# Optimization experiments

Measured on AMD Instinct MI355X. Metric: run time of the kernel, lower is better.

The kernel has to match this reference:

```python
import jax, jax.numpy as jnp
import numpy as np

EMBED_DIM = 512
N_HEADS = 8
HEAD_DIM = EMBED_DIM // N_HEADS
SEQ = 4096
BATCH = 2


def setup_inputs() -> dict:
    key = jax.random.key(0)
    k1, k2, k3 = jax.random.split(key, 3)
    x = jax.random.normal(k1, (SEQ, BATCH, EMBED_DIM), dtype=jnp.float32)
    # xavier_uniform for [3E, E]: limit = sqrt(6/(3E+E))
    lim_in = float(np.sqrt(6.0 / (3 * EMBED_DIM + EMBED_DIM)))
    in_proj_weight = jax.random.uniform(k2, (3 * EMBED_DIM, EMBED_DIM), minval=-lim_in, maxval=lim_in, dtype=jnp.float32)
    in_proj_bias = jnp.zeros((3 * EMBED_DIM,), jnp.float32)
    lim_out = float(np.sqrt(1.0 / EMBED_DIM))  # torch Linear default init range
    out_weight = jax.random.uniform(k3, (EMBED_DIM, EMBED_DIM), minval=-lim_out, maxval=lim_out, dtype=jnp.float32)
    out_bias = jnp.zeros((EMBED_DIM,), jnp.float32)
    return {"x": x, "in_proj_weight": in_proj_weight, "in_proj_bias": in_proj_bias,
            "out_weight": out_weight, "out_bias": out_bias}


def reference(x, in_proj_weight, in_proj_bias, out_weight, out_bias):
    # x: [S, B, E] (seq-first, as in the torch module)
    S, B, E = x.shape
    H, D = N_HEADS, HEAD_DIM
    scaling = 1.0 / (D ** 0.5)
    qkv = x @ in_proj_weight.T + in_proj_bias            # [S, B, 3E]
    q, k, v = jnp.split(qkv, 3, axis=-1)                 # each [S, B, E]
    # reshape to [B*H, S, D]
    def to_bh(t):
        return t.reshape(S, B * H, D).transpose(1, 0, 2)
    q = to_bh(q * scaling)
    k = to_bh(k)
    v = to_bh(v)
    scores = jnp.einsum('bqd,bkd->bqk', q, k)            # [B*H, S, S]
    attn = jax.nn.softmax(scores, axis=-1)
    out = jnp.einsum('bqk,bkd->bqd', attn, v)            # [B*H, S, D]
    out = out.transpose(1, 0, 2).reshape(S, B, E)        # [S, B, E]
    return out @ out_weight.T + out_bias
```

## Files before the change

kernel.cpp:

```cpp
#include <hip/hip_runtime.h>

typedef unsigned short u16;
typedef unsigned int   u32;
typedef short bf16x8 __attribute__((ext_vector_type(8)));
typedef float f32x2  __attribute__((ext_vector_type(2)));
typedef float f32x4  __attribute__((ext_vector_type(4)));
typedef float f32x16 __attribute__((ext_vector_type(16)));
typedef u32   u32x4  __attribute__((ext_vector_type(4)));

#define QK_SCALE 0.18033688011112042f

__device__ __forceinline__ u16 f2bf(float f) {
  u32 u = __builtin_bit_cast(u32, f);
  u = (u + 0x7FFFu + ((u >> 16) & 1u)) >> 16;
  return (u16)u;
}

__device__ __forceinline__ u32 cvtpk(float lo, float hi) {
  u32 r;
  asm("v_cvt_pk_bf16_f32 %0, %1, %2" : "=v"(r) : "v"(lo), "v"(hi));
  return r;
}

__device__ __forceinline__ void gload16(void* lds, const void* g) {
  __builtin_amdgcn_global_load_lds(
      (const __attribute__((address_space(1))) u32*)g,
      (__attribute__((address_space(3))) u32*)lds, 16, 0, 0);
}

__device__ __forceinline__ bf16x8 ld8(const void* p) {
  return *(const bf16x8*)p;
}

__global__ __launch_bounds__(256) void cvt_kernel(
    const float* __restrict__ x, const float* __restrict__ w1,
    const float* __restrict__ w2,
    u16* __restrict__ xb, u16* __restrict__ wb, u16* __restrict__ ob) {
  int i = blockIdx.x * 256 + threadIdx.x;
  const float* src; u16* dst; int off;
  if (i < 1048576)            { src = x;  dst = xb; off = i; }
  else if (i < 1048576+196608){ src = w1; dst = wb; off = i - 1048576; }
  else                        { src = w2; dst = ob; off = i - 1245184; }
  float4 v = ((const float4*)src)[off];
  ushort4 o;
  o.x = f2bf(v.x); o.y = f2bf(v.y); o.z = f2bf(v.z); o.w = f2bf(v.w);
  ((ushort4*)dst)[off] = o;
}

template<int MODE>
__global__ __launch_bounds__(256, 2) void gemm_bt(
    const u16* __restrict__ A, const u16* __restrict__ Bm,
    const float* __restrict__ bias,
    u16* __restrict__ q_out, u16* __restrict__ k_out, u16* __restrict__ v_out,
    float* __restrict__ f_out, int M, int N, int K) {
  __shared__ __attribute__((aligned(16))) u16 As[128 * 64];
  __shared__ __attribute__((aligned(16))) u16 Bs[128 * 64];
  const int tid = threadIdx.x, lane = tid & 63, w = tid >> 6;
  const int wm = w >> 1, wn = w & 1;
  const int lo = lane & 15, hi = lane >> 4;
  const int m0 = blockIdx.x * 128, n0 = blockIdx.y * 128;
  f32x4 acc[4][4] = {};
  const int srow = lane >> 3;
  const int skc  = (lane & 7) ^ srow;
  const int nk = K >> 6;
  for (int kt = 0; kt < nk; ++kt) {
    __syncthreads();
    const int k0 = kt * 64;
#pragma unroll
    for (int c = 0; c < 4; ++c) {
      const int ch = w * 4 + c;
      const int row = ch * 8 + srow;
      gload16((char*)As + ch * 1024, A  + (size_t)(m0 + row) * K + k0 + skc * 8);
      gload16((char*)Bs + ch * 1024, Bm + (size_t)(n0 + row) * K + k0 + skc * 8);
    }
    __syncthreads();
#pragma unroll
    for (int kk = 0; kk < 2; ++kk) {
      bf16x8 af[4], bfr[4];
#pragma unroll
      for (int mi = 0; mi < 4; ++mi) {
        const int row = wm * 64 + mi * 16 + lo;
        const int kc = kk * 4 + hi;
        af[mi] = ld8((const char*)As + row * 128 + ((kc ^ (row & 7)) << 4));
      }
#pragma unroll
      for (int ni = 0; ni < 4; ++ni) {
        const int row = wn * 64 + ni * 16 + lo;
        const int kc = kk * 4 + hi;
        bfr[ni] = ld8((const char*)Bs + row * 128 + ((kc ^ (row & 7)) << 4));
      }
#pragma unroll
      for (int mi = 0; mi < 4; ++mi)
#pragma unroll
        for (int ni = 0; ni < 4; ++ni)
          acc[mi][ni] = __builtin_amdgcn_mfma_f32_16x16x32_bf16(
              af[mi], bfr[ni], acc[mi][ni], 0, 0, 0);
    }
  }
#pragma unroll
  for (int mi = 0; mi < 4; ++mi)
#pragma unroll
    for (int ni = 0; ni < 4; ++ni) {
      const int gn = n0 + wn * 64 + ni * 16 + lo;
      const float bv = bias[gn];
#pragma unroll
      for (int r = 0; r < 4; ++r) {
        const int gm = m0 + wm * 64 + mi * 16 + hi * 4 + r;
        float val = acc[mi][ni][r] + bv;
        if (MODE == 0) {
          const int s = gm >> 1, b = gm & 1;
          const int sec = gn >> 9, e = gn & 511;
          const int h = e >> 6, d = e & 63;
          const size_t o = (((size_t)(b * 8 + h) * 4096 + s) << 6) + d;
          if (sec == 0)      q_out[o] = f2bf(val * QK_SCALE);
          else if (sec == 1) k_out[o] = f2bf(val);
          else               v_out[o] = f2bf(val);
        } else {
          f_out[(size_t)gm * N + gn] = val;
        }
      }
    }
}

__global__ __launch_bounds__(256) void transpose_v(
    const u16* __restrict__ v, u16* __restrict__ vt) {
  __shared__ __attribute__((aligned(16))) u16 T[64 * 72];
  const int bh = blockIdx.y, s0 = blockIdx.x * 64;
  const int t = threadIdx.x;
#pragma unroll
  for (int i = 0; i < 2; ++i) {
    const int idx = t + i * 256;
    const int row = idx >> 3, c = idx & 7;
    uint4 d = *(const uint4*)(v + ((size_t)bh * 4096 + s0 + row) * 64 + c * 8);
    *(uint4*)(&T[row * 72 + c * 8]) = d;
  }
  __syncthreads();
#pragma unroll
  for (int i = 0; i < 2; ++i) {
    const int idx = t + i * 256;
    const int dcol = idx >> 3, sc = idx & 7;
    u16 tmp[8];
#pragma unroll
    for (int j = 0; j < 8; ++j) tmp[j] = T[(sc * 8 + j) * 72 + dcol];
    *(uint4*)(vt + ((size_t)bh * 64 + dcol) * 4096 + s0 + sc * 8) = *(const uint4*)tmp;
  }
}

__global__ __launch_bounds__(256, 2) void fa_kernel(
    const u16* __restrict__ q, const u16* __restrict__ k,
    const u16* __restrict__ vt, u16* __restrict__ attn) {
  __shared__ __attribute__((aligned(16))) char S_lds[2][2][16384];
  __shared__ float Ml[2][2][32];
  const int tid = threadIdx.x, lane = tid & 63, w = tid >> 6;
  const int lo = lane & 31, hi5 = lane >> 5;
  const int wq = w & 1;
  const int kvh = w >> 1;
  const int wg = blockIdx.x;
  const int xcd = wg & 7, idx = wg >> 3;
  const int bh = xcd * 2 + (idx >> 5), qb = idx & 31;
  const int q0 = qb * 128 + wq * 64;
  const size_t hb = (size_t)bh * 4096 * 64;
  const u16* kbase = k + hb;
  const u16* vbase = vt + hb;
  bf16x8 qfA[4], qfB[4];
#pragma unroll
  for (int ds = 0; ds < 4; ++ds) {
    qfA[ds] = ld8(q + hb + (size_t)(q0 + lo) * 64 + ds * 16 + hi5 * 8);
    qfB[ds] = ld8(q + hb + (size_t)(q0 + 32 + lo) * 64 + ds * 16 + hi5 * 8);
  }

  f32x16 accA[2] = {}, accB[2] = {};
  float lrunA = 0.f, lrunB = 0.f;
  bf16x8 paA[4], paB[4];
  bf16x8 vfr[8];

  const int srow8 = lane >> 3;
  const int sx    = (lane & 7) ^ srow8;
  const int schunk = wq * 4;

#define STAGE(buf, kv0)                                                       \
  {                                                                           \
    char* kb_l = S_lds[kvh][buf];                                             \
    char* vb_l = kb_l + 8192;                                                 \
    _Pragma("unroll")                                                         \
    for (int i = 0; i < 4; ++i) {                                             \
      const int c = schunk + i;                       \
      gload16(kb_l + c * 1024,                                                \
              kbase + (size_t)((kv0) + c * 8 + srow8) * 64 + sx * 8);         \
      gload16(vb_l + c * 1024,                                                \
              vbase + (size_t)(c * 8 + srow8) * 4096 + (kv0) + sx * 8);       \
    }                                                                         \
  }

#define PACK(stv, ksl, pa)                                                    \
  {                                                                           \
    u32 A0 = cvtpk(stv[8 * ksl + 0], stv[8 * ksl + 1]);                       \
    u32 A1 = cvtpk(stv[8 * ksl + 2], stv[8 * ksl + 3]);                       \
    u32 B0 = cvtpk(stv[8 * ksl + 4], stv[8 * ksl + 5]);                       \
    u32 B1 = cvtpk(stv[8 * ksl + 6], stv[8 * ksl + 7]);                       \
    asm("v_permlane32_swap_b32 %0, %1" : "+v"(A0), "+v"(B0));                 \
    asm("v_permlane32_swap_b32 %0, %1" : "+v"(A1), "+v"(B1));                 \
    u32x4 pw; pw.x = A0; pw.y = A1; pw.z = B0; pw.w = B1;                     \
    pa = __builtin_bit_cast(bf16x8, pw);                                      \
  }

#define PVSTEP()                                                              \
  {                                                                           \
    __builtin_amdgcn_s_setprio(1);                                            \
    _Pragma("unroll")                                                         \
    for (int sl = 0; sl < 4; ++sl)                                            \
      _Pragma("unroll")                                                       \
      for (int ds2 = 0; ds2 < 2; ++ds2) {                                     \
        accA[ds2] = __builtin_amdgcn_mfma_f32_32x32x16_bf16(                  \
            paA[sl], vfr[sl * 2 + ds2], accA[ds2], 0, 0, 0);                  \
        accB[ds2] = __builtin_amdgcn_mfma_f32_32x32x16_bf16(                  \
            paB[sl], vfr[sl * 2 + ds2], accB[ds2], 0, 0, 0);                  \
      }                                                                       \
    __builtin_amdgcn_s_setprio(0);                                            \
  }

#define COMPUTE(CUR)                                                          \
  {                                                                           \
    const char* kl = S_lds[kvh][CUR];                                         \
    const char* vl = kl + 8192;                                               \
    f32x16 stA0 = {}, stA1 = {}, stB0 = {}, stB1 = {};                        \
    __builtin_amdgcn_s_setprio(1);                                            \
    _Pragma("unroll")                                                         \
    for (int ds = 0; ds < 4; ++ds) {                                          \
      const int r0 = lo, r1 = 32 + lo;                                        \
      const int col = ds * 32 + hi5 * 16;                                     \
      bf16x8 kf0 = ld8(kl + r0 * 128 + (col ^ ((r0 & 7) << 4)));              \
      bf16x8 kf1 = ld8(kl + r1 * 128 + (col ^ ((r1 & 7) << 4)));              \
      stA0 = __builtin_amdgcn_mfma_f32_32x32x16_bf16(kf0, qfA[ds], stA0,0,0,0);\
      stB0 = __builtin_amdgcn_mfma_f32_32x32x16_bf16(kf0, qfB[ds], stB0,0,0,0);\
      stA1 = __builtin_amdgcn_mfma_f32_32x32x16_bf16(kf1, qfA[ds], stA1,0,0,0);\
      stB1 = __builtin_amdgcn_mfma_f32_32x32x16_bf16(kf1, qfB[ds], stB1,0,0,0);\
    }                                                                         \
    __builtin_amdgcn_s_setprio(0);                                            \
    _Pragma("unroll")                                                         \
    for (int sl = 0; sl < 4; ++sl)                                            \
      _Pragma("unroll")                                                       \
      for (int ds2 = 0; ds2 < 2; ++ds2) {                                     \
        const int row = ds2 * 32 + lo;                                        \
        vfr[sl * 2 + ds2] = ld8(vl + row * 128 +                              \
                                ((sl * 32 + hi5 * 16) ^ ((row & 7) << 4)));   \
      }                                                                       \
    f32x2 ltA; ltA.x = 0.f; ltA.y = 0.f;                                      \
    f32x2 ltB; ltB.x = 0.f; ltB.y = 0.f;                                      \
    _Pragma("unroll")                                                         \
    for (int i = 0; i < 8; ++i) {                                             \
      stA0[2*i]   = __builtin_amdgcn_exp2f(stA0[2*i]);                        \
      stA0[2*i+1] = __builtin_amdgcn_exp2f(stA0[2*i+1]);                      \
      f32x2 a0; a0.x = stA0[2*i]; a0.y = stA0[2*i+1]; ltA += a0;              \
      stA1[2*i]   = __builtin_amdgcn_exp2f(stA1[2*i]);                        \
      stA1[2*i+1] = __builtin_amdgcn_exp2f(stA1[2*i+1]);                      \
      f32x2 a1; a1.x = stA1[2*i]; a1.y = stA1[2*i+1]; ltA += a1;              \
      stB0[2*i]   = __builtin_amdgcn_exp2f(stB0[2*i]);                        \
      stB0[2*i+1] = __builtin_amdgcn_exp2f(stB0[2*i+1]);                      \
      f32x2 b0; b0.x = stB0[2*i]; b0.y = stB0[2*i+1]; ltB += b0;              \
      stB1[2*i]   = __builtin_amdgcn_exp2f(stB1[2*i]);                        \
      stB1[2*i+1] = __builtin_amdgcn_exp2f(stB1[2*i+1]);                      \
      f32x2 b1; b1.x = stB1[2*i]; b1.y = stB1[2*i+1]; ltB += b1;              \
    }                                                                         \
    lrunA += ltA.x + ltA.y;                                                   \
    lrunB += ltB.x + ltB.y;                                                   \
    PACK(stA0, 0, paA[0]); PACK(stA0, 1, paA[1]);                             \
    PACK(stA1, 0, paA[2]); PACK(stA1, 1, paA[3]);                             \
    PACK(stB0, 0, paB[0]); PACK(stB0, 1, paB[1]);                             \
    PACK(stB1, 0, paB[2]); PACK(stB1, 1, paB[3]);                             \
  }

  const int kvbase = kvh * 2048;
  STAGE(0, kvbase);
  __syncthreads();
  STAGE(1, kvbase + 64);
  COMPUTE(0);
  __syncthreads();

  for (int t = 1; t < 32; ++t) {
    const int cur = t & 1;
    if (t < 31) STAGE(cur ^ 1, kvbase + (t + 1) * 64);
    PVSTEP();
    if (cur) { COMPUTE(1); } else { COMPUTE(0); }
    __syncthreads();
  }
  PVSTEP();

  lrunA += __shfl_xor(lrunA, 32);
  lrunB += __shfl_xor(lrunB, 32);
  float* Ob = (float*)S_lds;
  if (w >= 2) {
#pragma unroll
    for (int r = 0; r < 16; ++r) {
      const int crow = (r & 3) + 8 * (r >> 2) + 4 * hi5;
#pragma unroll
      for (int ds2 = 0; ds2 < 2; ++ds2) {
        Ob[((wq * 2 + 0) * 32 + crow) * 64 + ds2 * 32 + lo] = accA[ds2][r];
        Ob[((wq * 2 + 1) * 32 + crow) * 64 + ds2 * 32 + lo] = accB[ds2][r];
      }
    }
    if (hi5 == 0) { Ml[wq][0][lo] = lrunA; Ml[wq][1][lo] = lrunB; }
  }
  __syncthreads();
  if (w < 2) {
    const float linvA = 1.0f / (lrunA + Ml[wq][0][lo]);
    const float linvB = 1.0f / (lrunB + Ml[wq][1][lo]);
    const int b = bh >> 3, h = bh & 7;
#pragma unroll
    for (int r = 0; r < 16; ++r) {
      const int crow = (r & 3) + 8 * (r >> 2) + 4 * hi5;
      const float ivA = __shfl(linvA, crow);
      const float ivB = __shfl(linvB, crow);
      const int sA = q0 + crow, sB = q0 + 32 + crow;
#pragma unroll
      for (int ds2 = 0; ds2 < 2; ++ds2) {
        const float oA = Ob[((wq * 2 + 0) * 32 + crow) * 64 + ds2 * 32 + lo];
        const float oB = Ob[((wq * 2 + 1) * 32 + crow) * 64 + ds2 * 32 + lo];
        attn[(size_t)(sA * 2 + b) * 512 + h * 64 + ds2 * 32 + lo] =
            f2bf((accA[ds2][r] + oA) * ivA);
        attn[(size_t)(sB * 2 + b) * 512 + h * 64 + ds2 * 32 + lo] =
            f2bf((accB[ds2][r] + oB) * ivB);
      }
    }
  }
#undef STAGE
#undef PACK
#undef PVSTEP
#undef COMPUTE
}

extern "C" void kernel_launch(void* const* d_in, const int* in_sizes, int n_in,
                              void* d_out, int out_size, void* d_ws, size_t ws_size,
                              hipStream_t stream) {
  const float* x     = (const float*)d_in[0];
  const float* w_in  = (const float*)d_in[1];
  const float* b_in  = (const float*)d_in[2];
  const float* w_out = (const float*)d_in[3];
  const float* b_out = (const float*)d_in[4];
  float* out = (float*)d_out;
  char* ws = (char*)d_ws;
  u16* xb  = (u16*)(ws);
  u16* wb  = (u16*)(ws + 8388608);
  u16* ob  = (u16*)(ws + 9961472);
  u16* qb  = (u16*)(ws + 10485760);
  u16* kb  = (u16*)(ws + 18874368);
  u16* vb  = (u16*)(ws + 27262976);
  u16* vtb = (u16*)(ws + 35651584);
  u16* attn = xb;

  cvt_kernel<<<5120, 256, 0, stream>>>(x, w_in, w_out, xb, wb, ob);
  gemm_bt<0><<<dim3(64, 12), 256, 0, stream>>>(xb, wb, b_in, qb, kb, vb,
                                               nullptr, 8192, 1536, 512);
  transpose_v<<<dim3(64, 16), 256, 0, stream>>>(vb, vtb);
  fa_kernel<<<512, 256, 0, stream>>>(qb, kb, vtb, attn);
  gemm_bt<1><<<dim3(64, 4), 256, 0, stream>>>(attn, ob, b_out, nullptr, nullptr,
                                              nullptr, out, 8192, 512, 512);
}
```

Baseline: 132.4 us.

## Halve FA query tile per wave and ping-pong two score tiles across KV steps

The attention kernel now gives each wave 32 query rows instead of 64 and doubles the grid to 1024 workgroups. The main loop alternates between even and odd score/V-fragment register sets, so the QK^T MFMAs for the next KV block can overlap the exp/pack/PV work of the previous one. The aim is better occupancy and latency hiding. In exchange, each K/V tile staged in LDS is reused by half as many query rows, which doubles K/V global traffic. An extra barrier is also added before the epilogue reuses LDS.

```diff
diff --git a/kernel.cpp b/kernel.cpp
--- a/kernel.cpp
+++ b/kernel.cpp
@@ -31,6 +31,8 @@
 __device__ __forceinline__ bf16x8 ld8(const void* p) {
   return *(const bf16x8*)p;
 }
+
+__device__ __forceinline__ f32x16 fz16() { f32x16 z = {}; return z; }
 
 __global__ __launch_bounds__(256) void cvt_kernel(
     const float* __restrict__ x, const float* __restrict__ w1,
@@ -150,29 +152,27 @@
     const u16* __restrict__ q, const u16* __restrict__ k,
     const u16* __restrict__ vt, u16* __restrict__ attn) {
   __shared__ __attribute__((aligned(16))) char S_lds[2][2][16384];
-  __shared__ float Ml[2][2][32];
+  __shared__ float Ml[2][32];
   const int tid = threadIdx.x, lane = tid & 63, w = tid >> 6;
   const int lo = lane & 31, hi5 = lane >> 5;
   const int wq = w & 1;
   const int kvh = w >> 1;
   const int wg = blockIdx.x;
   const int xcd = wg & 7, idx = wg >> 3;
-  const int bh = xcd * 2 + (idx >> 5), qb = idx & 31;
-  const int q0 = qb * 128 + wq * 64;
+  const int bh = xcd * 2 + (idx >> 6), qb = idx & 63;
+  const int q0 = qb * 64 + wq * 32;
   const size_t hb = (size_t)bh * 4096 * 64;
   const u16* kbase = k + hb;
   const u16* vbase = vt + hb;
-  bf16x8 qfA[4], qfB[4];
-#pragma unroll
-  for (int ds = 0; ds < 4; ++ds) {
-    qfA[ds] = ld8(q + hb + (size_t)(q0 + lo) * 64 + ds * 16 + hi5 * 8);
-    qfB[ds] = ld8(q + hb + (size_t)(q0 + 32 + lo) * 64 + ds * 16 + hi5 * 8);
-  }
-
-  f32x16 accA[2] = {}, accB[2] = {};
-  float lrunA = 0.f, lrunB = 0.f;
-  bf16x8 paA[4], paB[4];
-  bf16x8 vfr[8];
+  bf16x8 qf[4];
+#pragma unroll
+  for (int ds = 0; ds < 4; ++ds)
+    qf[ds] = ld8(q + hb + (size_t)(q0 + lo) * 64 + ds * 16 + hi5 * 8);
+
+  f32x16 acc[2] = {};
+  float lrun = 0.f;
+  f32x16 stE0, stE1, stO0, stO1;
+  bf16x8 vfE[8], vfO[8];
 
   const int srow8 = lane >> 3;
   const int sx    = (lane & 7) ^ srow8;
@@ -204,129 +204,116 @@
     pa = __builtin_bit_cast(bf16x8, pw);                                      \
   }
 
-#define PVSTEP()                                                              \
-  {                                                                           \
-    __builtin_amdgcn_s_setprio(1);                                            \
-    _Pragma("unroll")                                                         \
-    for (int sl = 0; sl < 4; ++sl)                                            \
-      _Pragma("unroll")                                                       \
-      for (int ds2 = 0; ds2 < 2; ++ds2) {                                     \
-        accA[ds2] = __builtin_amdgcn_mfma_f32_32x32x16_bf16(                  \
-            paA[sl], vfr[sl * 2 + ds2], accA[ds2], 0, 0, 0);                  \
-        accB[ds2] = __builtin_amdgcn_mfma_f32_32x32x16_bf16(                  \
-            paB[sl], vfr[sl * 2 + ds2], accB[ds2], 0, 0, 0);                  \
-      }                                                                       \
-    __builtin_amdgcn_s_setprio(0);                                            \
-  }
-
-#define COMPUTE(CUR)                                                          \
+#define PRODUCE(CUR, S0, S1, VF)                                              \
   {                                                                           \
     const char* kl = S_lds[kvh][CUR];                                         \
     const char* vl = kl + 8192;                                               \
-    f32x16 stA0 = {}, stA1 = {}, stB0 = {}, stB1 = {};                        \
-    __builtin_amdgcn_s_setprio(1);                                            \
+    S0 = fz16(); S1 = fz16();                                                 \
     _Pragma("unroll")                                                         \
     for (int ds = 0; ds < 4; ++ds) {                                          \
       const int r0 = lo, r1 = 32 + lo;                                        \
       const int col = ds * 32 + hi5 * 16;                                     \
       bf16x8 kf0 = ld8(kl + r0 * 128 + (col ^ ((r0 & 7) << 4)));              \
       bf16x8 kf1 = ld8(kl + r1 * 128 + (col ^ ((r1 & 7) << 4)));              \
-      stA0 = __builtin_amdgcn_mfma_f32_32x32x16_bf16(kf0, qfA[ds], stA0,0,0,0);\
-      stB0 = __builtin_amdgcn_mfma_f32_32x32x16_bf16(kf0, qfB[ds], stB0,0,0,0);\
-      stA1 = __builtin_amdgcn_mfma_f32_32x32x16_bf16(kf1, qfA[ds], stA1,0,0,0);\
-      stB1 = __builtin_amdgcn_mfma_f32_32x32x16_bf16(kf1, qfB[ds], stB1,0,0,0);\
+      S0 = __builtin_amdgcn_mfma_f32_32x32x16_bf16(kf0, qf[ds], S0, 0, 0, 0); \
+      S1 = __builtin_amdgcn_mfma_f32_32x32x16_bf16(kf1, qf[ds], S1, 0, 0, 0); \
     }                                                                         \
-    __builtin_amdgcn_s_setprio(0);                                            \
     _Pragma("unroll")                                                         \
     for (int sl = 0; sl < 4; ++sl)                                            \
       _Pragma("unroll")                                                       \
       for (int ds2 = 0; ds2 < 2; ++ds2) {                                     \
         const int row = ds2 * 32 + lo;                                        \
-        vfr[sl * 2 + ds2] = ld8(vl + row * 128 +                              \
-                                ((sl * 32 + hi5 * 16) ^ ((row & 7) << 4)));   \
+        VF[sl * 2 + ds2] = ld8(vl + row * 128 +                               \
+                               ((sl * 32 + hi5 * 16) ^ ((row & 7) << 4)));    \
       }                                                                       \
-    f32x2 ltA; ltA.x = 0.f; ltA.y = 0.f;                                      \
-    f32x2 ltB; ltB.x = 0.f; ltB.y = 0.f;                                      \
+  }
+
+#define CONSUME(S0, S1, VF)                                                   \
+  {                                                                           \
+    f32x2 lt; lt.x = 0.f; lt.y = 0.f;                                         \
     _Pragma("unroll")                                                         \
     for (int i = 0; i < 8; ++i) {                                             \
-      stA0[2*i]   = __builtin_amdgcn_exp2f(stA0[2*i]);                        \
-      stA0[2*i+1] = __builtin_amdgcn_exp2f(stA0[2*i+1]);                      \
-      f32x2 a0; a0.x = stA0[2*i]; a0.y = stA0[2*i+1]; ltA += a0;              \
-      stA1[2*i]   = __builtin_amdgcn_exp2f(stA1[2*i]);                        \
-      stA1[2*i+1] = __builtin_amdgcn_exp2f(stA1[2*i+1]);                      \
-      f32x2 a1; a1.x = stA1[2*i]; a1.y = stA1[2*i+1]; ltA += a1;              \
-      stB0[2*i]   = __builtin_amdgcn_exp2f(stB0[2*i]);                        \
-      stB0[2*i+1] = __builtin_amdgcn_exp2f(stB0[2*i+1]);                      \
-      f32x2 b0; b0.x = stB0[2*i]; b0.y = stB0[2*i+1]; ltB += b0;              \
-      stB1[2*i]   = __builtin_amdgcn_exp2f(stB1[2*i]);                        \
-      stB1[2*i+1] = __builtin_amdgcn_exp2f(stB1[2*i+1]);                      \
-      f32x2 b1; b1.x = stB1[2*i]; b1.y = stB1[2*i+1]; ltB += b1;              \
+      S0[2*i]   = __builtin_amdgcn_exp2f(S0[2*i]);                            \
+      S0[2*i+1] = __builtin_amdgcn_exp2f(S0[2*i+1]);                          \
+      f32x2 e0; e0.x = S0[2*i]; e0.y = S0[2*i+1]; lt += e0;                   \
+      S1[2*i]   = __builtin_amdgcn_exp2f(S1[2*i]);                            \
+      S1[2*i+1] = __builtin_amdgcn_exp2f(S1[2*i+1]);                          \
+      f32x2 e1; e1.x = S1[2*i]; e1.y = S1[2*i+1]; lt += e1;                   \
     }                                                                         \
-    lrunA += ltA.x + ltA.y;                                                   \
-    lrunB += ltB.x + ltB.y;                                                   \
-    PACK(stA0, 0, paA[0]); PACK(stA0, 1, paA[1]);                             \
-    PACK(stA1, 0, paA[2]); PACK(stA1, 1, paA[3]);                             \
-    PACK(stB0, 0, paB[0]); PACK(stB0, 1, paB[1]);                             \
-    PACK(stB1, 0, paB[2]); PACK(stB1, 1, paB[3]);                             \
+    lrun += lt.x + lt.y;                                                      \
+    bf16x8 pa0, pa1, pa2, pa3;                                                \
+    PACK(S0, 0, pa0); PACK(S0, 1, pa1);                                       \
+    PACK(S1, 0, pa2); PACK(S1, 1, pa3);                                       \
+    __builtin_amdgcn_s_setprio(1);                                            \
+    _Pragma("unroll")                                                         \
+    for (int ds2 = 0; ds2 < 2; ++ds2) {                                       \
+      acc[ds2] = __builtin_amdgcn_mfma_f32_32x32x16_bf16(pa0, VF[0 + ds2],    \
+                                                         acc[ds2], 0, 0, 0); \
+      acc[ds2] = __builtin_amdgcn_mfma_f32_32x32x16_bf16(pa1, VF[2 + ds2],    \
+                                                         acc[ds2], 0, 0, 0); \
+      acc[ds2] = __builtin_amdgcn_mfma_f32_32x32x16_bf16(pa2, VF[4 + ds2],    \
+                                                         acc[ds2], 0, 0, 0); \
+      acc[ds2] = __builtin_amdgcn_mfma_f32_32x32x16_bf16(pa3, VF[6 + ds2],    \
+                                                         acc[ds2], 0, 0, 0); \
+    }                                                                         \
+    __builtin_amdgcn_s_setprio(0);                                            \
   }
 
   const int kvbase = kvh * 2048;
   STAGE(0, kvbase);
   __syncthreads();
   STAGE(1, kvbase + 64);
-  COMPUTE(0);
-  __syncthreads();
-
-  for (int t = 1; t < 32; ++t) {
-    const int cur = t & 1;
-    if (t < 31) STAGE(cur ^ 1, kvbase + (t + 1) * 64);
-    PVSTEP();
-    if (cur) { COMPUTE(1); } else { COMPUTE(0); }
+  PRODUCE(0, stE0, stE1, vfE);
+  __syncthreads();
+
+  for (int t = 1; t < 31; t += 2) {
+    STAGE(0, kvbase + (t + 1) * 64);
+    PRODUCE(1, stO0, stO1, vfO);
+    CONSUME(stE0, stE1, vfE);
     __syncthreads();
-  }
-  PVSTEP();
-
-  lrunA += __shfl_xor(lrunA, 32);
-  lrunB += __shfl_xor(lrunB, 32);
+    STAGE(1, kvbase + (t + 2) * 64);
+    PRODUCE(0, stE0, stE1, vfE);
+    CONSUME(stO0, stO1, vfO);
+    __syncthreads();
+  }
+  PRODUCE(1, stO0, stO1, vfO);
+  CONSUME(stE0, stE1, vfE);
+  CONSUME(stO0, stO1, vfO);
+
+  lrun += __shfl_xor(lrun, 32);
+  __syncthreads();
   float* Ob = (float*)S_lds;
   if (w >= 2) {
 #pragma unroll
     for (int r = 0; r < 16; ++r) {
       const int crow = (r & 3) + 8 * (r >> 2) + 4 * hi5;
 #pragma unroll
-      for (int ds2 = 0; ds2 < 2; ++ds2) {
-        Ob[((wq * 2 + 0) * 32 + crow) * 64 + ds2 * 32 + lo] = accA[ds2][r];
-        Ob[((wq * 2 + 1) * 32 + crow) * 64 + ds2 * 32 + lo] = accB[ds2][r];
-      }
-    }
-    if (hi5 == 0) { Ml[wq][0][lo] = lrunA; Ml[wq][1][lo] = lrunB; }
+      for (int ds2 = 0; ds2 < 2; ++ds2)
+        Ob[(wq * 32 + crow) * 64 + ds2 * 32 + lo] = acc[ds2][r];
+    }
+    if (hi5 == 0) Ml[wq][lo] = lrun;
   }
   __syncthreads();
   if (w < 2) {
-    const float linvA = 1.0f / (lrunA + Ml[wq][0][lo]);
-    const float linvB = 1.0f / (lrunB + Ml[wq][1][lo]);
+    const float linv = 1.0f / (lrun + Ml[wq][lo]);
     const int b = bh >> 3, h = bh & 7;
 #pragma unroll
     for (int r = 0; r < 16; ++r) {
       const int crow = (r & 3) + 8 * (r >> 2) + 4 * hi5;
-      const float ivA = __shfl(linvA, crow);
-      const float ivB = __shfl(linvB, crow);
-      const int sA = q0 + crow, sB = q0 + 32 + crow;
+      const float ivR = __shfl(linv, crow);
+      const int s = q0 + crow;
 #pragma unroll
       for (int ds2 = 0; ds2 < 2; ++ds2) {
-        const float oA = Ob[((wq * 2 + 0) * 32 + crow) * 64 + ds2 * 32 + lo];
-        const float oB = Ob[((wq * 2 + 1) * 32 + crow) * 64 + ds2 * 32 + lo];
-        attn[(size_t)(sA * 2 + b) * 512 + h * 64 + ds2 * 32 + lo] =
-            f2bf((accA[ds2][r] + oA) * ivA);
-        attn[(size_t)(sB * 2 + b) * 512 + h * 64 + ds2 * 32 + lo] =
-            f2bf((accB[ds2][r] + oB) * ivB);
+        const float ob = Ob[(wq * 32 + crow) * 64 + ds2 * 32 + lo];
+        attn[(size_t)(s * 2 + b) * 512 + h * 64 + ds2 * 32 + lo] =
+            f2bf((acc[ds2][r] + ob) * ivR);
       }
     }
   }
 #undef STAGE
 #undef PACK
-#undef PVSTEP
-#undef COMPUTE
+#undef PRODUCE
+#undef CONSUME
 }
 
 extern "C" void kernel_launch(void* const* d_in, const int* in_sizes, int n_in,
@@ -352,7 +339,7 @@
   gemm_bt<0><<<dim3(64, 12), 256, 0, stream>>>(xb, wb, b_in, qb, kb, vb,
                                                nullptr, 8192, 1536, 512);
   transpose_v<<<dim3(64, 16), 256, 0, stream>>>(vb, vtb);
-  fa_kernel<<<512, 256, 0, stream>>>(qb, kb, vtb, attn);
+  fa_kernel<<<1024, 256, 0, stream>>>(qb, kb, vtb, attn);
   gemm_bt<1><<<dim3(64, 4), 256, 0, stream>>>(attn, ob, b_out, nullptr, nullptr,
                                               nullptr, out, 8192, 512, 512);
 }
```

Result: slower. 139.2 us (+5.1%).
